# Performance work log

Hardware: AMD Instinct MI355X
Metric: run time of the kernel (lower is better)

Reference implementation:

```python
import jax, jax.numpy as jnp
import numpy as np

N = 1024  # num boxes (labels == predictions count so diff == 0 branch)


def jaccard(box_a, box_b):
    # box_a: [A,4], box_b: [B,4], xyxy format -> IoU matrix [A,B]
    max_xy = jnp.minimum(box_a[:, None, 2:], box_b[None, :, 2:])
    min_xy = jnp.maximum(box_a[:, None, :2], box_b[None, :, :2])
    inter_wh = jnp.clip(max_xy - min_xy, 0.0)
    inter = inter_wh[..., 0] * inter_wh[..., 1]
    area_a = ((box_a[:, 2] - box_a[:, 0]) * (box_a[:, 3] - box_a[:, 1]))[:, None]
    area_b = ((box_b[:, 2] - box_b[:, 0]) * (box_b[:, 3] - box_b[:, 1]))[None, :]
    return inter / (area_a + area_b - inter)


def greedy_match(JM):
    """Replicates the original greedy loop: N steps; each step takes the LAST
    row-major-order maximal entry ('>=' update) among rows/cols not in `seen`,
    swaps label rows r<->c (tracked via perm), and marks column c as seen."""
    n = JM.shape[0]
    MASKED = jnp.float32(-1.0)  # IoU >= 0, so -1 excludes masked entries

    def body(carry, _):
        perm, seen = carry
        M = JM[perm]                                  # rows permuted with labels
        mask = seen[:, None] | seen[None, :]          # one `seen` set for rows & cols
        vals = jnp.where(mask, MASKED, M).reshape(-1)
        # last occurrence of the max (the '>=' in the Python loop keeps the latest)
        i = vals.shape[0] - 1 - jnp.argmax(vals[::-1])
        r, c = i // n, i % n
        pr, pc = perm[r], perm[c]
        perm = perm.at[r].set(pc).at[c].set(pr)
        seen = seen.at[c].set(True)
        return (perm, seen), None

    init = (jnp.arange(n), jnp.zeros(n, dtype=bool))
    (perm, _), _ = jax.lax.scan(body, init, None, length=n)
    return perm


def setup_inputs() -> dict:
    key = jax.random.key(0)
    k1, k2, k3, k4, k5 = jax.random.split(key, 5)
    # valid xyxy boxes: x2 > x1, y2 > y1
    lmin = jax.random.uniform(k1, (N, 2), dtype=jnp.float32)
    lwh = jax.random.uniform(k2, (N, 2), dtype=jnp.float32) * 0.2 + 0.01
    labels = jnp.concatenate([lmin, lmin + lwh], axis=-1)
    pmin = jax.random.uniform(k3, (N, 2), dtype=jnp.float32)
    pwh = jax.random.uniform(k4, (N, 2), dtype=jnp.float32) * 0.2 + 0.01
    predictions = jnp.concatenate([pmin, pmin + pwh], axis=-1)
    scores = jax.random.normal(k5, (N,), dtype=jnp.float32)
    return {"predictions": predictions, "labels": labels, "scores": scores}


def reference(predictions, labels, scores):
    # L == P -> diff == 0, no truncation, scores untouched.
    JM = jaccard(labels, predictions)
    perm = greedy_match(JM)
    labels_matched = labels[perm]
    # F.l1_loss default reduction: mean over all elements.
    # NOTE: the original's `loss.add(F.cross_entropy(...))` is non-in-place and
    # its result is discarded, so the CE term does NOT contribute; diff == 0 so
    # the diff*4 branch is skipped. Faithfully: loss = L1 only.
    loss = jnp.mean(jnp.abs(labels_matched - predictions))
    return loss
```

## Files before the change

### kernel.cpp

```cpp
#include <hip/hip_runtime.h>
#include <stdint.h>

#define NBOX 1024
#define UNK  0xFFFFFFFFFFFFFFFFull

typedef unsigned long long u64;
typedef unsigned int u32;
typedef unsigned short u16;
typedef unsigned char u8;

__device__ __forceinline__ float iou_pair(const float4 lb, float larea,
                                          const float4 pb, float parea) {
    float ix1 = fmaxf(lb.x, pb.x);
    float iy1 = fmaxf(lb.y, pb.y);
    float ix2 = fminf(lb.z, pb.z);
    float iy2 = fminf(lb.w, pb.w);
    float w = fmaxf(__fsub_rn(ix2, ix1), 0.0f);
    float h = fmaxf(__fsub_rn(iy2, iy1), 0.0f);
    float inter = __fmul_rn(w, h);
    float denom = __fsub_rn(__fadd_rn(larea, parea), inter);
    return inter / denom;
}

__device__ __forceinline__ u64 umax64(u64 a, u64 b) { return a > b ? a : b; }
__device__ __forceinline__ u64 umin64(u64 a, u64 b) { return a < b ? a : b; }

__device__ __forceinline__ u64 dpp_max64(u64 v) {
    unsigned lo, hi; u64 o;
#define DPP_STEP(CTRL) \
    lo = (unsigned)__builtin_amdgcn_update_dpp(0, (int)(unsigned)(v & 0xffffffffull), CTRL, 0xf, 0xf, true); \
    hi = (unsigned)__builtin_amdgcn_update_dpp(0, (int)(unsigned)(v >> 32),           CTRL, 0xf, 0xf, true); \
    o = (((u64)hi) << 32) | lo; \
    if (o > v) v = o;
    DPP_STEP(0x111) DPP_STEP(0x112) DPP_STEP(0x114)
    DPP_STEP(0x118) DPP_STEP(0x142) DPP_STEP(0x143)
#undef DPP_STEP
    return v;
}

__device__ __forceinline__ void dpp_top2(u64 &a1, u64 &a2) {
    unsigned lo, hi; u64 b1, b2, min1;
#define T2STEP(CTRL) \
    lo = (unsigned)__builtin_amdgcn_update_dpp(0, (int)(unsigned)(a1 & 0xffffffffull), CTRL, 0xf, 0xf, true); \
    hi = (unsigned)__builtin_amdgcn_update_dpp(0, (int)(unsigned)(a1 >> 32),           CTRL, 0xf, 0xf, true); \
    b1 = (((u64)hi) << 32) | lo; \
    lo = (unsigned)__builtin_amdgcn_update_dpp(0, (int)(unsigned)(a2 & 0xffffffffull), CTRL, 0xf, 0xf, true); \
    hi = (unsigned)__builtin_amdgcn_update_dpp(0, (int)(unsigned)(a2 >> 32),           CTRL, 0xf, 0xf, true); \
    b2 = (((u64)hi) << 32) | lo; \
    min1 = (b1 == a1) ? 0ull : umin64(a1, b1); \
    a1 = umax64(a1, b1); \
    a2 = umax64(umax64(a2, b2), min1);
    T2STEP(0x111) T2STEP(0x112) T2STEP(0x114) T2STEP(0x118) T2STEP(0x142) T2STEP(0x143)
#undef T2STEP
}

__device__ __forceinline__ u64 readlane64(u64 v, int l) {
    unsigned lo = (unsigned)__builtin_amdgcn_readlane((int)(unsigned)(v & 0xffffffffull), l);
    unsigned hi = (unsigned)__builtin_amdgcn_readlane((int)(unsigned)(v >> 32), l);
    return (((u64)hi) << 32) | lo;
}
__device__ __forceinline__ u32 readlane32(u32 v, int l) {
    return (u32)__builtin_amdgcn_readlane((int)v, l);
}

#define SHR_T2_STEP(a1, a2, CTRL) { \
    unsigned _lo, _hi; u64 _b1, _b2, _mn; \
    _lo = (unsigned)__builtin_amdgcn_update_dpp(0, (int)(unsigned)((a1) & 0xffffffffull), CTRL, 0xf, 0xf, true); \
    _hi = (unsigned)__builtin_amdgcn_update_dpp(0, (int)(unsigned)((a1) >> 32),           CTRL, 0xf, 0xf, true); \
    _b1 = (((u64)_hi) << 32) | _lo; \
    _lo = (unsigned)__builtin_amdgcn_update_dpp(0, (int)(unsigned)((a2) & 0xffffffffull), CTRL, 0xf, 0xf, true); \
    _hi = (unsigned)__builtin_amdgcn_update_dpp(0, (int)(unsigned)((a2) >> 32),           CTRL, 0xf, 0xf, true); \
    _b2 = (((u64)_hi) << 32) | _lo; \
    _mn = umin64((a1), _b1); \
    (a1) = umax64((a1), _b1); \
    (a2) = umax64(umax64((a2), _b2), _mn); }

#define SHR_V2_STEP(v1, v2, CTRL) { \
    u32 _s1 = (u32)__builtin_amdgcn_update_dpp(0, (int)(v1), CTRL, 0xf, 0xf, true); \
    u32 _s2 = (u32)__builtin_amdgcn_update_dpp(0, (int)(v2), CTRL, 0xf, 0xf, true); \
    u32 _mn = (v1) < _s1 ? (v1) : _s1; \
    (v1) = (v1) > _s1 ? (v1) : _s1; \
    u32 _m2 = (v2) > _s2 ? (v2) : _s2; \
    (v2) = _m2 > _mn ? _m2 : _mn; }

__global__ void __launch_bounds__(64) jm_init(const float* __restrict__ labels,
                                              const float* __restrict__ preds,
                                              float* __restrict__ JM,
                                              u64* __restrict__ rkey_ws,
                                              u64* __restrict__ rkey2_ws) {
    const int b = blockIdx.x;
    const int lane = threadIdx.x;
    float4 lb = ((const float4*)labels)[b];
    float la = __fmul_rn(__fsub_rn(lb.z, lb.x), __fsub_rn(lb.w, lb.y));
    u64 a1 = 0, a2 = 0;
    #pragma unroll
    for (int m = 0; m < 4; ++m) {
        float4 v;
        float* vv = (float*)&v;
        #pragma unroll
        for (int k = 0; k < 4; ++k) {
            int c = 4 * lane + 256 * m + k;
            float4 pb = ((const float4*)preds)[c];
            float pa = __fmul_rn(__fsub_rn(pb.z, pb.x), __fsub_rn(pb.w, pb.y));
            vv[k] = iou_pair(lb, la, pb, pa);
        }
        if (JM) ((float4*)JM)[b * 256 + lane + 64 * m] = v;
        #pragma unroll
        for (int k = 0; k < 4; ++k) {
            int c = 4 * lane + 256 * m + k;
            u64 p = ((u64)__float_as_uint(vv[k]) << 10) | (unsigned)c;
            a2 = umax64(a2, umin64(a1, p));
            a1 = umax64(a1, p);
        }
    }
    dpp_top2(a1, a2);
    if (lane == 63) {
        if ((a1 >> 10) == 0ull) { rkey_ws[b] = 0ull; rkey2_ws[b] = 0ull; }
        else { rkey_ws[b] = a1; rkey2_ws[b] = (a2 >> 10) ? a2 : 0ull; }
    }
}

__global__ void __launch_bounds__(64) init_colmax(const float* __restrict__ labels,
                                                  const float* __restrict__ preds,
                                                  float* __restrict__ JMT,
                                                  u64* __restrict__ cub_ws) {
    const int c = blockIdx.x;
    const int lane = threadIdx.x;
    float4 pc = ((const float4*)preds)[c];
    float pa = __fmul_rn(__fsub_rn(pc.z, pc.x), __fsub_rn(pc.w, pc.y));
    u64 best = 0; u32 v1 = 0, v2 = 0;
    #pragma unroll
    for (int j = 0; j < 16; ++j) {
        int L = lane + (j << 6);
        float4 lb = ((const float4*)labels)[L];
        float la = __fmul_rn(__fsub_rn(lb.z, lb.x), __fsub_rn(lb.w, lb.y));
        float v = iou_pair(lb, la, pc, pa);
        if (JMT) JMT[(size_t)c * NBOX + L] = v;
        u32 vb = __float_as_uint(v);
        if (vb >= v1) { v2 = v1; v1 = vb; } else { v2 = (vb > v2) ? vb : v2; }
        best = umax64(best, ((u64)vb << 10) | (unsigned)L);
    }
    best = dpp_max64(best);
    u64 bm = readlane64(best, 63);
    u32 V = (u32)(bm >> 10);
    u64 b1 = __ballot(v1 == V);
    u64 b2 = __ballot(v2 == V);
    bool tie = (__popcll(b1) >= 2) || (b2 != 0ull);
    if (lane == 63)
        cub_ws[c] = V ? (((u64)V << 32) | (tie ? (1ull << 16) : 0ull) | (bm & 1023ull))
                      : 0ull;
}

__global__ void __launch_bounds__(1024, 1)
rounds_kernel(const float* __restrict__ preds,
              const float* __restrict__ labels,
              const float* __restrict__ JM,
              const float* __restrict__ JMT,
              const u64* __restrict__ rkey_ws,
              const u64* __restrict__ rkey2_ws,
              const u64* __restrict__ cub_ws,
              float* __restrict__ out) {
    __shared__ float4 pred4s[NBOX];
    __shared__ float4 lab4s[NBOX];
    __shared__ float  parea_s[NBOX];
    __shared__ float  larea_s[NBOX];
    __shared__ u64    rkey[NBOX];
    __shared__ u64    rkey2[NBOX];
    __shared__ u64    cub[NBOX];
    __shared__ u64    colbest[NBOX];
    __shared__ u16    pos_s[NBOX];
    __shared__ u16    dest_s[NBOX];
    __shared__ u16    perm_s[NBOX];
    __shared__ u8     seenc[NBOX];
    __shared__ u8     lockedl[NBOX];
    __shared__ u32    seenw[32];
    __shared__ u32    lockedw[32];
    __shared__ int    ncommit;
    __shared__ float  fpart[16];

    const int t    = (int)threadIdx.x;
    const int lane = t & 63;
    const int wid  = t >> 6;

    {
        float4 p = ((const float4*)preds)[t];
        float4 L = ((const float4*)labels)[t];
        pred4s[t] = p;
        lab4s[t]  = L;
        parea_s[t] = __fmul_rn(__fsub_rn(p.z, p.x), __fsub_rn(p.w, p.y));
        larea_s[t] = __fmul_rn(__fsub_rn(L.z, L.x), __fsub_rn(L.w, L.y));
        pos_s[t] = (u16)t; perm_s[t] = (u16)t; dest_s[t] = 0;
        seenc[t] = 0; lockedl[t] = 0;
        rkey[t]  = rkey_ws  ? rkey_ws[t]  : 0ull;
        rkey2[t] = rkey2_ws ? rkey2_ws[t] : UNK;
        cub[t]   = cub_ws   ? cub_ws[t]   : 0ull;
        colbest[t] = 0ull;
        if (t < 32) { seenw[t] = 0u; lockedw[t] = 0u; }
        if (t == 0) ncommit = 0;
    }
    __syncthreads();

    u32 myseen = 0;
    u32 mylocked = 0;

    auto scan_row2 = [&](int La, int Lb, bool hb,
                         u64 &r1a, u64 &r2a, u64 &r1b, u64 &r2b) {
        u32 av1 = 0, ac1 = 0, av2 = 0, ac2 = 0;
        u32 bv1 = 0, bc1 = 0, bv2 = 0, bc2 = 0;
        if (JM) {
            const float4* A4 = (const float4*)(JM + (size_t)La * NBOX);
            const float4* B4 = (const float4*)(JM + (size_t)Lb * NBOX);
            #pragma unroll
            for (int m = 0; m < 4; ++m) {
                float4 fa = A4[lane + 64 * m];
                float4 fb = B4[lane + 64 * m];
                const float* qa = (const float*)&fa;
                const float* qb = (const float*)&fb;
                #pragma unroll
                for (int k = 0; k < 4; ++k) {
                    u32 cc = (u32)(4 * lane + 256 * m + k);
                    bool msk = (myseen >> ((m << 2) | k)) & 1u;
                    u32 va = __float_as_uint(qa[k]);
                    u32 vb = __float_as_uint(qb[k]);
                    if (!msk && va) {
                        if (va >= av1) { av2 = av1; ac2 = ac1; av1 = va; ac1 = cc; }
                        else if (va >= av2) { av2 = va; ac2 = cc; }
                    }
                    if (!msk && vb) {
                        if (vb >= bv1) { bv2 = bv1; bc2 = bc1; bv1 = vb; bc1 = cc; }
                        else if (vb >= bv2) { bv2 = vb; bc2 = cc; }
                    }
                }
            }
        } else {
            float4 lba = lab4s[La]; float laa = larea_s[La];
            float4 lbb = lab4s[Lb]; float lbb_a = larea_s[Lb];
            #pragma unroll
            for (int m = 0; m < 4; ++m) {
                #pragma unroll
                for (int k = 0; k < 4; ++k) {
                    u32 cc = (u32)(4 * lane + 256 * m + k);
                    bool msk = (myseen >> ((m << 2) | k)) & 1u;
                    u32 va = __float_as_uint(iou_pair(lba, laa, pred4s[cc], parea_s[cc]));
                    u32 vb = __float_as_uint(iou_pair(lbb, lbb_a, pred4s[cc], parea_s[cc]));
                    if (!msk && va) {
                        if (va >= av1) { av2 = av1; ac2 = ac1; av1 = va; ac1 = cc; }
                        else if (va >= av2) { av2 = va; ac2 = cc; }
                    }
                    if (!msk && vb) {
                        if (vb >= bv1) { bv2 = bv1; bc2 = bc1; bv1 = vb; bc1 = cc; }
                        else if (vb >= bv2) { bv2 = vb; bc2 = cc; }
                    }
                }
            }
        }
        u64 a1 = ((u64)av1 << 10) | ac1, a2 = ((u64)av2 << 10) | ac2;
        u64 b1 = ((u64)bv1 << 10) | bc1, b2 = ((u64)bv2 << 10) | bc2;
        SHR_T2_STEP(a1, a2, 0x111) SHR_T2_STEP(b1, b2, 0x111)
        SHR_T2_STEP(a1, a2, 0x112) SHR_T2_STEP(b1, b2, 0x112)
        SHR_T2_STEP(a1, a2, 0x114) SHR_T2_STEP(b1, b2, 0x114)
        SHR_T2_STEP(a1, a2, 0x118) SHR_T2_STEP(b1, b2, 0x118)
        {
            u64 p1 = readlane64(a1, 15), p2 = readlane64(a2, 15);
            u64 q1 = readlane64(a1, 31), q2 = readlane64(a2, 31);
            u64 s1 = readlane64(a1, 47), s2 = readlane64(a2, 47);
            u64 w1 = readlane64(a1, 63), w2 = readlane64(a2, 63);
            u64 mn = umin64(p1, q1); p1 = umax64(p1, q1); p2 = umax64(umax64(p2, q2), mn);
            mn = umin64(s1, w1); s1 = umax64(s1, w1); s2 = umax64(umax64(s2, w2), mn);
            mn = umin64(p1, s1); p1 = umax64(p1, s1); p2 = umax64(umax64(p2, s2), mn);
            r1a = p1; r2a = p2;
        }
        if (hb) {
            u64 p1 = readlane64(b1, 15), p2 = readlane64(b2, 15);
            u64 q1 = readlane64(b1, 31), q2 = readlane64(b2, 31);
            u64 s1 = readlane64(b1, 47), s2 = readlane64(b2, 47);
            u64 w1 = readlane64(b1, 63), w2 = readlane64(b2, 63);
            u64 mn = umin64(p1, q1); p1 = umax64(p1, q1); p2 = umax64(umax64(p2, q2), mn);
            mn = umin64(s1, w1); s1 = umax64(s1, w1); s2 = umax64(umax64(s2, w2), mn);
            mn = umin64(p1, s1); p1 = umax64(p1, s1); p2 = umax64(umax64(p2, s2), mn);
            r1b = p1; r2b = p2;
        } else { r1b = 0; r2b = 0; }
    };

    auto store_rkey = [&](int L, u64 r1, u64 r2) {
        if (lane == 0) {
            if ((r1 >> 10) == 0ull) { rkey[L] = 0ull; rkey2[L] = 0ull; }
            else { rkey[L] = r1; rkey2[L] = (r2 >> 10) ? r2 : 0ull; }
        }
    };

    auto scan_col_exact = [&](int c) -> u64 {
        u64 best = 0; u32 v1 = 0, v2 = 0;
        if (JMT) {
            const float4* col4 = (const float4*)(JMT + (size_t)c * NBOX);
            #pragma unroll
            for (int m = 0; m < 4; ++m) {
                float4 f = col4[lane + 64 * m];
                const float* ff = (const float*)&f;
                #pragma unroll
                for (int k = 0; k < 4; ++k) {
                    int L = 4 * lane + 256 * m + k;
                    u32 vb = __float_as_uint(ff[k]);
                    if ((mylocked >> ((m << 2) | k)) & 1u) vb = 0;
                    if (vb >= v1) { v2 = v1; v1 = vb; } else { v2 = (vb > v2) ? vb : v2; }
                    u64 key = ((u64)vb << 20) | ((u64)pos_s[L] << 10) | (unsigned)L;
                    if (!vb) key = 0;
                    best = umax64(best, key);
                }
            }
        } else {
            float4 pc = pred4s[c];
            float  pa = parea_s[c];
            #pragma unroll
            for (int m = 0; m < 4; ++m) {
                #pragma unroll
                for (int k = 0; k < 4; ++k) {
                    int L = 4 * lane + 256 * m + k;
                    float v = iou_pair(lab4s[L], larea_s[L], pc, pa);
                    u32 vb = __float_as_uint(v);
                    if ((mylocked >> ((m << 2) | k)) & 1u) vb = 0;
                    if (vb >= v1) { v2 = v1; v1 = vb; } else { v2 = (vb > v2) ? vb : v2; }
                    u64 key = ((u64)vb << 20) | ((u64)pos_s[L] << 10) | (unsigned)L;
                    if (!vb) key = 0;
                    best = umax64(best, key);
                }
            }
        }
        best = dpp_max64(best);
        u64 bm = readlane64(best, 63);
        u32 V = (u32)(bm >> 20);
        u64 b1 = __ballot(v1 == V);
        u64 b2 = __ballot(v2 == V);
        bool tie = (__popcll(b1) >= 2) || (b2 != 0ull);
        return V ? (((u64)V << 32) | (tie ? (1ull << 16) : 0ull) | (bm & 1023ull)) : 0ull;
    };

    auto scan_col2 = [&](int ca, int cb, bool hb, u64 &oa, u64 &ob) {
        u32 av1 = 0, av2 = 0, al1 = 0;
        u32 bv1 = 0, bv2 = 0, bl1 = 0;
        if (JMT) {
            const float4* A4 = (const float4*)(JMT + (size_t)ca * NBOX);
            const float4* B4 = (const float4*)(JMT + (size_t)cb * NBOX);
            #pragma unroll
            for (int m = 0; m < 4; ++m) {
                float4 fa = A4[lane + 64 * m];
                float4 fb = B4[lane + 64 * m];
                const float* qa = (const float*)&fa;
                const float* qb = (const float*)&fb;
                #pragma unroll
                for (int k = 0; k < 4; ++k) {
                    u32 L = (u32)(4 * lane + 256 * m + k);
                    bool msk = (mylocked >> ((m << 2) | k)) & 1u;
                    u32 va = msk ? 0u : __float_as_uint(qa[k]);
                    u32 vb = msk ? 0u : __float_as_uint(qb[k]);
                    if (va > av1) { av2 = av1; av1 = va; al1 = L; }
                    else av2 = (va > av2) ? va : av2;
                    if (vb > bv1) { bv2 = bv1; bv1 = vb; bl1 = L; }
                    else bv2 = (vb > bv2) ? vb : bv2;
                }
            }
        } else {
            float4 pca = pred4s[ca]; float paa = parea_s[ca];
            float4 pcb = pred4s[cb]; float pab = parea_s[cb];
            #pragma unroll
            for (int m = 0; m < 4; ++m) {
                #pragma unroll
                for (int k = 0; k < 4; ++k) {
                    u32 L = (u32)(4 * lane + 256 * m + k);
                    bool msk = (mylocked >> ((m << 2) | k)) & 1u;
                    u32 va = msk ? 0u : __float_as_uint(iou_pair(lab4s[L], larea_s[L], pca, paa));
                    u32 vb = msk ? 0u : __float_as_uint(iou_pair(lab4s[L], larea_s[L], pcb, pab));
                    if (va > av1) { av2 = av1; av1 = va; al1 = L; }
                    else av2 = (va > av2) ? va : av2;
                    if (vb > bv1) { bv2 = bv1; bv1 = vb; bl1 = L; }
                    else bv2 = (vb > bv2) ? vb : bv2;
                }
            }
        }
        u32 sva = av1, sla = al1;
        u32 svb = bv1, slb = bl1;
        SHR_V2_STEP(av1, av2, 0x111) SHR_V2_STEP(bv1, bv2, 0x111)
        SHR_V2_STEP(av1, av2, 0x112) SHR_V2_STEP(bv1, bv2, 0x112)
        SHR_V2_STEP(av1, av2, 0x114) SHR_V2_STEP(bv1, bv2, 0x114)
        SHR_V2_STEP(av1, av2, 0x118) SHR_V2_STEP(bv1, bv2, 0x118)
        u32 Va, V2a, Vb, V2b;
        {
            u32 p1 = readlane32(av1, 15), p2 = readlane32(av2, 15);
            u32 q1 = readlane32(av1, 31), q2 = readlane32(av2, 31);
            u32 s1 = readlane32(av1, 47), s2 = readlane32(av2, 47);
            u32 w1 = readlane32(av1, 63), w2 = readlane32(av2, 63);
            u32 mn = p1 < q1 ? p1 : q1; p1 = p1 > q1 ? p1 : q1;
            p2 = p2 > q2 ? p2 : q2; p2 = p2 > mn ? p2 : mn;
            mn = s1 < w1 ? s1 : w1; s1 = s1 > w1 ? s1 : w1;
            s2 = s2 > w2 ? s2 : w2; s2 = s2 > mn ? s2 : mn;
            mn = p1 < s1 ? p1 : s1; p1 = p1 > s1 ? p1 : s1;
            p2 = p2 > s2 ? p2 : s2; p2 = p2 > mn ? p2 : mn;
            Va = p1; V2a = p2;
        }
        {
            u32 p1 = readlane32(bv1, 15), p2 = readlane32(bv2, 15);
            u32 q1 = readlane32(bv1, 31), q2 = readlane32(bv2, 31);
            u32 s1 = readlane32(bv1, 47), s2 = readlane32(bv2, 47);
            u32 w1 = readlane32(bv1, 63), w2 = readlane32(bv2, 63);
            u32 mn = p1 < q1 ? p1 : q1; p1 = p1 > q1 ? p1 : q1;
            p2 = p2 > q2 ? p2 : q2; p2 = p2 > mn ? p2 : mn;
            mn = s1 < w1 ? s1 : w1; s1 = s1 > w1 ? s1 : w1;
            s2 = s2 > w2 ? s2 : w2; s2 = s2 > mn ? s2 : mn;
            mn = p1 < s1 ? p1 : s1; p1 = p1 > s1 ? p1 : s1;
            p2 = p2 > s2 ? p2 : s2; p2 = p2 > mn ? p2 : mn;
            Vb = p1; V2b = p2;
        }
        if (Va == 0) oa = 0ull;
        else if (V2a == Va) oa = UNK;
        else {
            u64 ball = __ballot(sva == Va);
            int wl = (int)__ffsll(ball) - 1;
            u32 lbl = readlane32(sla, wl);
            oa = ((u64)Va << 32) | lbl;
        }
        if (!hb) { ob = 0ull; return; }
        if (Vb == 0) ob = 0ull;
        else if (V2b == Vb) ob = UNK;
        else {
            u64 ball = __ballot(svb == Vb);
            int wl = (int)__ffsll(ball) - 1;
            u32 lbl = readlane32(slb, wl);
            ob = ((u64)Vb << 32) | lbl;
        }
    };

    auto try_commit = [&](int c, u64 cbv) {
        u64 sb = colbest[c];
        if (sb && cbv && !((cbv >> 16) & 1ull) &&
            (u32)(cbv & 1023ull) == (u32)(sb & 1023ull)) {
            int L = (int)(sb & 1023ull);
            seenc[c] = 1; lockedl[L] = 1; rkey[L] = 0ull;
            dest_s[L] = (u16)c; perm_s[c] = (u16)L;
            atomicOr(&seenw[c >> 5], 1u << (c & 31));
            atomicOr(&lockedw[L >> 5], 1u << (L & 31));
            atomicAdd(&ncommit, 1);
        }
    };

    if (!rkey_ws) {
        for (int L = 2 * wid; L < NBOX; L += 32) {
            u64 r1a, r2a, r1b, r2b;
            scan_row2(L, L + 1, true, r1a, r2a, r1b, r2b);
            store_rkey(L, r1a, r2a);
            store_rkey(L + 1, r1b, r2b);
        }
        for (int c = 2 * wid; c < NBOX; c += 32) {
            u64 oa, ob;
            scan_col2(c, c + 1, true, oa, ob);
            if (oa == UNK) oa = scan_col_exact(c);
            if (ob == UNK) ob = scan_col_exact(c + 1);
            if (lane == 0) { cub[c] = oa; cub[c + 1] = ob; }
        }
        __syncthreads();
    }

    for (int round = 0; round < 2048; ++round) {
        {
            u64 k = rkey[t];
            if (k) atomicMax((unsigned long long*)&colbest[k & 1023ull],
                             ((k >> 10) << 20) | ((u64)pos_s[t] << 10) | (u64)(unsigned)t);
            if (t == 0) ncommit = 0;
        }
        __syncthreads();

        {
            bool need = false;
            u64 sb = colbest[t];
            if (sb) {
                u32 sval = (u32)(sb >> 20);
                u32 slab = (u32)(sb & 1023ull);
                u64 cb = cub[t];
                u32 cval = (u32)(cb >> 32);
                u32 clab = (u32)(cb & 1023ull);
                bool ctie = (cb >> 16) & 1ull;
                if (lockedl[clab] || ctie || (sval == cval && slab != clab)) {
                    need = true;
                } else if (slab == clab) {
                    int c = t, L = (int)slab;
                    seenc[c] = 1; lockedl[L] = 1; rkey[L] = 0ull;
                    dest_s[L] = (u16)c; perm_s[c] = (u16)L;
                    atomicOr(&seenw[c >> 5], 1u << (c & 31));
                    atomicOr(&lockedw[L >> 5], 1u << (L & 31));
                    atomicAdd(&ncommit, 1);
                }
            }
            u64 bal = __ballot(need);
            while (bal) {
                int l0 = (int)__ffsll(bal) - 1; bal &= bal - 1;
                int l1 = l0; bool hb = false;
                if (bal) { l1 = (int)__ffsll(bal) - 1; bal &= bal - 1; hb = true; }
                int c0 = (wid << 6) | l0, c1 = (wid << 6) | l1;
                u64 o0, o1;
                scan_col2(c0, c1, hb, o0, o1);
                if (o0 == UNK) o0 = scan_col_exact(c0);
                if (hb && o1 == UNK) o1 = scan_col_exact(c1);
                if (lane == 0) {
                    cub[c0] = o0; try_commit(c0, o0);
                    if (hb) { cub[c1] = o1; try_commit(c1, o1); }
                }
            }
        }
        __syncthreads();

        const int nc = ncommit;
        {
            u32 ms = 0, ml = 0;
            #pragma unroll
            for (int m = 0; m < 4; ++m) {
                u32 ws_ = seenw[(lane >> 3) + (m << 3)];
                u32 wl  = lockedw[(lane >> 3) + (m << 3)];
                u32 sh  = (lane & 7) << 2;
                ms |= ((ws_ >> sh) & 0xFu) << (m << 2);
                ml |= ((wl  >> sh) & 0xFu) << (m << 2);
            }
            myseen = ms; mylocked = ml;
        }
        {
            bool needrow = false;
            u64 k = rkey[t];
            if (k && seenc[k & 1023ull]) {
                u64 k2 = rkey2[t];
                if (k2 != UNK) {
                    rkey[t] = k2;
                    rkey2[t] = UNK;
                    if (k2 && seenc[k2 & 1023ull]) needrow = true;
                } else {
                    needrow = true;
                }
            }
            u64 bal = __ballot(needrow);
            while (bal) {
                int l0 = (int)__ffsll(bal) - 1; bal &= bal - 1;
                int l1 = l0; bool hb = false;
                if (bal) { l1 = (int)__ffsll(bal) - 1; bal &= bal - 1; hb = true; }
                int r0 = (wid << 6) | l0, r1_ = (wid << 6) | l1;
                u64 r1a, r2a, r1b, r2b;
                scan_row2(r0, r1_, hb, r1a, r2a, r1b, r2b);
                store_rkey(r0, r1a, r2a);
                if (hb) store_rkey(r1_, r1b, r2b);
            }
        }
        colbest[t] = 0ull;
        if (!seenc[t]) {
            int l = (int)perm_s[t];
            while (lockedl[l]) l = (int)dest_s[l];
            pos_s[l] = (u16)t;
            perm_s[t] = (u16)l;
        }
        __syncthreads();

        if (nc == 0) break;
    }

    {
        float4 lb = lab4s[perm_s[t]];
        float4 pb = pred4s[t];
        float sum = fabsf(lb.x - pb.x) + fabsf(lb.y - pb.y) +
                    fabsf(lb.z - pb.z) + fabsf(lb.w - pb.w);
        for (int off = 32; off > 0; off >>= 1) sum += __shfl_xor(sum, off, 64);
        if (lane == 0) fpart[wid] = sum;
        __syncthreads();
        if (t == 0) {
            float s = 0.0f;
            for (int w = 0; w < 16; ++w) s += fpart[w];
            out[0] = s * (1.0f / 4096.0f);
        }
    }
}

extern "C" void kernel_launch(void* const* d_in, const int* in_sizes, int n_in,
                              void* d_out, int out_size, void* d_ws, size_t ws_size,
                              hipStream_t stream) {
    const float* preds  = (const float*)d_in[0];
    const float* labels = (const float*)d_in[1];
    float* out = (float*)d_out;

    const size_t jm_b   = (size_t)NBOX * NBOX * sizeof(float);
    const size_t keys_b = 3 * NBOX * sizeof(u64);

    float *JM = nullptr, *JMT = nullptr;
    u64 *rk = nullptr, *rk2 = nullptr, *cb = nullptr;
    char* w = (char*)d_ws;

    if (d_ws && ws_size >= 2 * jm_b + keys_b) {
        JM  = (float*)w;
        JMT = (float*)(w + jm_b);
        rk  = (u64*)(w + 2 * jm_b); rk2 = rk + NBOX; cb = rk2 + NBOX;
    } else if (d_ws && ws_size >= jm_b + keys_b) {
        JM  = (float*)w;
        rk  = (u64*)(w + jm_b); rk2 = rk + NBOX; cb = rk2 + NBOX;
    } else if (d_ws && ws_size >= keys_b) {
        rk  = (u64*)w; rk2 = rk + NBOX; cb = rk2 + NBOX;
    }

    if (rk) {
        jm_init<<<NBOX, 64, 0, stream>>>(labels, preds, JM, rk, rk2);
        init_colmax<<<NBOX, 64, 0, stream>>>(labels, preds, JMT, cb);
    }
    rounds_kernel<<<1, 1024, 0, stream>>>(preds, labels, JM, JMT, rk, rk2, cb, out);
}
```

Baseline: 229.5 us.

## Merge colbest scatter into round tail and drop per-round position tracking

Drops the pos_s tie-break field from the column keys, so keys pack only value and label. The colbest atomicMax scatter moves to the end of each round, and the commit counter is double-buffered by round parity, which removes one __syncthreads per round. The permutation chase through dest_s now runs once after the loop instead of every round. This assumes that label index alone (without the position term) still picks the correct tie-break and that the deferred perm resolution matches the per-round updates.

```diff
diff --git a/kernel.cpp b/kernel.cpp
--- a/kernel.cpp
+++ b/kernel.cpp
@@ -168,14 +168,13 @@
     __shared__ u64    rkey2[NBOX];
     __shared__ u64    cub[NBOX];
     __shared__ u64    colbest[NBOX];
-    __shared__ u16    pos_s[NBOX];
     __shared__ u16    dest_s[NBOX];
     __shared__ u16    perm_s[NBOX];
     __shared__ u8     seenc[NBOX];
     __shared__ u8     lockedl[NBOX];
     __shared__ u32    seenw[32];
     __shared__ u32    lockedw[32];
-    __shared__ int    ncommit;
+    __shared__ int    ncom[2];
     __shared__ float  fpart[16];
 
     const int t    = (int)threadIdx.x;
@@ -189,19 +188,20 @@
         lab4s[t]  = L;
         parea_s[t] = __fmul_rn(__fsub_rn(p.z, p.x), __fsub_rn(p.w, p.y));
         larea_s[t] = __fmul_rn(__fsub_rn(L.z, L.x), __fsub_rn(L.w, L.y));
-        pos_s[t] = (u16)t; perm_s[t] = (u16)t; dest_s[t] = 0;
+        perm_s[t] = (u16)t; dest_s[t] = 0;
         seenc[t] = 0; lockedl[t] = 0;
         rkey[t]  = rkey_ws  ? rkey_ws[t]  : 0ull;
         rkey2[t] = rkey2_ws ? rkey2_ws[t] : UNK;
         cub[t]   = cub_ws   ? cub_ws[t]   : 0ull;
         colbest[t] = 0ull;
         if (t < 32) { seenw[t] = 0u; lockedw[t] = 0u; }
-        if (t == 0) ncommit = 0;
+        if (t < 2) ncom[t] = 0;
     }
     __syncthreads();
 
     u32 myseen = 0;
     u32 mylocked = 0;
+    int par = 0;
 
     auto scan_row2 = [&](int La, int Lb, bool hb,
                          u64 &r1a, u64 &r2a, u64 &r1b, u64 &r2b) {
@@ -303,9 +303,7 @@
                     u32 vb = __float_as_uint(ff[k]);
                     if ((mylocked >> ((m << 2) | k)) & 1u) vb = 0;
                     if (vb >= v1) { v2 = v1; v1 = vb; } else { v2 = (vb > v2) ? vb : v2; }
-                    u64 key = ((u64)vb << 20) | ((u64)pos_s[L] << 10) | (unsigned)L;
-                    if (!vb) key = 0;
-                    best = umax64(best, key);
+                    best = umax64(best, ((u64)vb << 10) | (unsigned)L);
                 }
             }
         } else {
@@ -320,15 +318,13 @@
                     u32 vb = __float_as_uint(v);
                     if ((mylocked >> ((m << 2) | k)) & 1u) vb = 0;
                     if (vb >= v1) { v2 = v1; v1 = vb; } else { v2 = (vb > v2) ? vb : v2; }
-                    u64 key = ((u64)vb << 20) | ((u64)pos_s[L] << 10) | (unsigned)L;
-                    if (!vb) key = 0;
-                    best = umax64(best, key);
+                    best = umax64(best, ((u64)vb << 10) | (unsigned)L);
                 }
             }
         }
         best = dpp_max64(best);
         u64 bm = readlane64(best, 63);
-        u32 V = (u32)(bm >> 20);
+        u32 V = (u32)(bm >> 10);
         u64 b1 = __ballot(v1 == V);
         u64 b2 = __ballot(v2 == V);
         bool tie = (__popcll(b1) >= 2) || (b2 != 0ull);
@@ -429,16 +425,15 @@
         }
     };
 
-    auto try_commit = [&](int c, u64 cbv) {
-        u64 sb = colbest[c];
-        if (sb && cbv && !((cbv >> 16) & 1ull) &&
-            (u32)(cbv & 1023ull) == (u32)(sb & 1023ull)) {
-            int L = (int)(sb & 1023ull);
+    auto try_commit = [&](int c, u64 cbv, u64 sb_) {
+        if (sb_ && cbv && !((cbv >> 16) & 1ull) &&
+            (u32)(cbv & 1023ull) == (u32)(sb_ & 1023ull)) {
+            int L = (int)(sb_ & 1023ull);
             seenc[c] = 1; lockedl[L] = 1; rkey[L] = 0ull;
             dest_s[L] = (u16)c; perm_s[c] = (u16)L;
             atomicOr(&seenw[c >> 5], 1u << (c & 31));
             atomicOr(&lockedw[L >> 5], 1u << (L & 31));
-            atomicAdd(&ncommit, 1);
+            atomicAdd(&ncom[par], 1);
         }
     };
 
@@ -459,20 +454,22 @@
         __syncthreads();
     }
 
+    {
+        u64 k = rkey[t];
+        if (k) atomicMax((unsigned long long*)&colbest[k & 1023ull],
+                         ((k >> 10) << 10) | (u64)(unsigned)t);
+    }
+    __syncthreads();
+
     for (int round = 0; round < 2048; ++round) {
+        par = round & 1;
+
         {
-            u64 k = rkey[t];
-            if (k) atomicMax((unsigned long long*)&colbest[k & 1023ull],
-                             ((k >> 10) << 20) | ((u64)pos_s[t] << 10) | (u64)(unsigned)t);
-            if (t == 0) ncommit = 0;
-        }
-        __syncthreads();
-
-        {
+            u64 sb = colbest[t];
+            colbest[t] = 0ull;
             bool need = false;
-            u64 sb = colbest[t];
             if (sb) {
-                u32 sval = (u32)(sb >> 20);
+                u32 sval = (u32)(sb >> 10);
                 u32 slab = (u32)(sb & 1023ull);
                 u64 cb = cub[t];
                 u32 cval = (u32)(cb >> 32);
@@ -486,7 +483,7 @@
                     dest_s[L] = (u16)c; perm_s[c] = (u16)L;
                     atomicOr(&seenw[c >> 5], 1u << (c & 31));
                     atomicOr(&lockedw[L >> 5], 1u << (L & 31));
-                    atomicAdd(&ncommit, 1);
+                    atomicAdd(&ncom[par], 1);
                 }
             }
             u64 bal = __ballot(need);
@@ -495,19 +492,23 @@
                 int l1 = l0; bool hb = false;
                 if (bal) { l1 = (int)__ffsll(bal) - 1; bal &= bal - 1; hb = true; }
                 int c0 = (wid << 6) | l0, c1 = (wid << 6) | l1;
+                u64 sb0 = readlane64(sb, l0);
+                u64 sb1 = hb ? readlane64(sb, l1) : 0ull;
                 u64 o0, o1;
                 scan_col2(c0, c1, hb, o0, o1);
                 if (o0 == UNK) o0 = scan_col_exact(c0);
                 if (hb && o1 == UNK) o1 = scan_col_exact(c1);
                 if (lane == 0) {
-                    cub[c0] = o0; try_commit(c0, o0);
-                    if (hb) { cub[c1] = o1; try_commit(c1, o1); }
+                    cub[c0] = o0; try_commit(c0, o0, sb0);
+                    if (hb) { cub[c1] = o1; try_commit(c1, o1, sb1); }
                 }
             }
         }
         __syncthreads();
 
-        const int nc = ncommit;
+        const int cnt = ncom[par];
+        if (t == 0) ncom[par ^ 1] = 0;
+        if (cnt == 0) break;
         {
             u32 ms = 0, ml = 0;
             #pragma unroll
@@ -545,17 +546,20 @@
                 if (hb) store_rkey(r1_, r1b, r2b);
             }
         }
-        colbest[t] = 0ull;
-        if (!seenc[t]) {
-            int l = (int)perm_s[t];
-            while (lockedl[l]) l = (int)dest_s[l];
-            pos_s[l] = (u16)t;
-            perm_s[t] = (u16)l;
+        {
+            u64 k = rkey[t];
+            if (k) atomicMax((unsigned long long*)&colbest[k & 1023ull],
+                             ((k >> 10) << 10) | (u64)(unsigned)t);
         }
         __syncthreads();
-
-        if (nc == 0) break;
-    }
+    }
+
+    if (!seenc[t]) {
+        int l = t;
+        while (lockedl[l]) l = (int)dest_s[l];
+        perm_s[t] = (u16)l;
+    }
+    __syncthreads();
 
     {
         float4 lb = lab4s[perm_s[t]];
```

Result: no change. 233.6 us (+1.8%).
